# Kernel tuning notes

Measured on AMD Instinct MI355X. Metric: run time of the kernel, lower is better.

Reference implementation:

```python
import jax, jax.numpy as jnp
import numpy as np

N_NODES = 100000
N_EDGES = 1600000
D_IN = 256
D_OUT = 128


def setup_inputs() -> dict:
    key = jax.random.key(0)
    k1, k2, k3, k4, k5, k6 = jax.random.split(key, 6)
    inp = {
        "input": jax.random.normal(k1, (N_NODES, D_IN), dtype=jnp.float32),
        "edge_row": jax.random.randint(k2, (N_EDGES,), 0, N_NODES),
        "edge_col": jax.random.randint(k3, (N_EDGES,), 0, N_NODES),
        "edge_val": jax.random.uniform(k4, (N_EDGES,), dtype=jnp.float32),
        "W": jax.random.normal(k5, (D_IN, D_OUT), dtype=jnp.float32) * (1.0 / np.sqrt(D_IN)),
        "b": jax.random.normal(k6, (D_OUT,), dtype=jnp.float32) * 0.01,
    }
    return inp


def reference(input, edge_row, edge_col, edge_val, W, b):
    # support = Linear(input)  -> [N, D_OUT]
    support = jnp.dot(input, W) + b
    # sparse.mm(adj, support): out[r] = sum_e val[e] * support[col[e]] for edges with row[e]==r
    msgs = edge_val[:, None] * support[edge_col]  # [E, D_OUT]
    agg = jax.ops.segment_sum(msgs, edge_row, num_segments=N_NODES)  # [N, D_OUT]
    return jnp.tanh(agg)
```

## Files before the change

kernel.cpp:

```cpp
#include <hip/hip_runtime.h>
#include <math.h>

#define N_NODES 100000
#define N_EDGES 1600000
#define D_IN 256
#define D_OUT 128

#define OFF_SUPPORT 0
#define OFF_COUNTS  51200000
#define OFF_CSREV   51600008
#define OFF_BSUMS   64400008
#define OFF_WTHI    64400416
#define OFF_WTLO    64465952

#define SCAN_CHUNK  1024
#define SCAN_BLOCKS ((N_NODES + SCAN_CHUNK - 1) / SCAN_CHUNK)

#define GB 128
#define GEMM_BLOCKS ((N_NODES + GB - 1) / GB)
#define EDGE_BLOCKS ((N_EDGES + 255) / 256)

typedef __attribute__((ext_vector_type(8))) short s8v;
typedef __attribute__((ext_vector_type(4))) float f4v;

__device__ __forceinline__ short f2bf(float x) {
  unsigned u = __float_as_uint(x);
  unsigned r = u + 0x7FFF + ((u >> 16) & 1);
  return (short)(r >> 16);
}
__device__ __forceinline__ float bf2f(short h) {
  return __uint_as_float(((unsigned)(unsigned short)h) << 16);
}

__device__ __forceinline__ void cvt8(float4 a, float4 b, s8v& h, s8v& l) {
  float f[8] = {a.x, a.y, a.z, a.w, b.x, b.y, b.z, b.w};
#pragma unroll
  for (int i = 0; i < 8; i++) {
    short hh = f2bf(f[i]);
    h[i] = hh;
    l[i] = f2bf(f[i] - bf2f(hh));
  }
}

typedef const float __attribute__((address_space(1)))* gas1f;
typedef float __attribute__((address_space(3)))* las3f;
__device__ __forceinline__ void gload_lds16(const float* g, float* l) {
  __builtin_amdgcn_global_load_lds((gas1f)g, (las3f)l, 16, 0, 0);
}

__global__ __launch_bounds__(256) void wconv_kernel(
    const float* __restrict__ W, short* __restrict__ wt_hi,
    short* __restrict__ wt_lo, int* __restrict__ counts) {
  int idx = blockIdx.x * 256 + threadIdx.x;
  int k = idx >> 7;
  int n = idx & 127;
  float v = W[idx];
  short h = f2bf(v);
  wt_hi[n * 256 + k] = h;
  wt_lo[n * 256 + k] = f2bf(v - bf2f(h));
  for (int i = idx; i < N_NODES + 1; i += 32768) counts[i] = 0;
}

__device__ __forceinline__ void gemm_body(
    int gb, const float* __restrict__ input, const short* __restrict__ wt_hi,
    const short* __restrict__ wt_lo, const float* __restrict__ b,
    float* __restrict__ support) {
  __shared__ float Af[4][2][32][32];
  const int t = threadIdx.x;
  const int lane = t & 63;
  const int wv = t >> 6;
  const int qm = lane & 15;
  const int quad = lane >> 4;
  const int node0 = gb * GB;

  const int srow = lane >> 3;
  const int gc = (lane & 7) ^ srow;

  auto stage = [&](int kt, int buf) {
#pragma unroll
    for (int j = 0; j < 4; ++j) {
      int nd = node0 + wv * 32 + j * 8 + srow;
      if (nd > N_NODES - 1) nd = N_NODES - 1;
      gload_lds16(input + (size_t)nd * D_IN + kt * 32 + gc * 4,
                  &Af[wv][buf][j * 8][0]);
    }
  };

  stage(0, 0);
  stage(1, 1);

  f4v acc[2][8];
#pragma unroll
  for (int mt = 0; mt < 2; mt++)
#pragma unroll
    for (int nt = 0; nt < 8; nt++) acc[mt][nt] = (f4v){0.f, 0.f, 0.f, 0.f};

  const int p0 = (2 * quad) ^ (qm & 7);
  const int p1 = (2 * quad + 1) ^ (qm & 7);

#pragma unroll
  for (int kt = 0; kt < 8; ++kt) {
    const int cb = kt & 1;
    asm volatile("s_waitcnt vmcnt(4)" ::: "memory");
    float4 x00 = *(const float4*)&Af[wv][cb][qm][p0 * 4];
    float4 x01 = *(const float4*)&Af[wv][cb][qm][p1 * 4];
    float4 x10 = *(const float4*)&Af[wv][cb][qm + 16][p0 * 4];
    float4 x11 = *(const float4*)&Af[wv][cb][qm + 16][p1 * 4];
    asm volatile("s_waitcnt lgkmcnt(0)" ::: "memory");
    __builtin_amdgcn_sched_barrier(0);

    const int koff = kt * 32 + quad * 8;
    s8v bh[8], bl[8];
#pragma unroll
    for (int nt = 0; nt < 8; ++nt) {
      size_t bo = (size_t)(nt * 16 + qm) * 256 + koff;
      bh[nt] = *(const s8v*)(wt_hi + bo);
      bl[nt] = *(const s8v*)(wt_lo + bo);
    }
    __builtin_amdgcn_sched_barrier(0);
    if (kt < 6) stage(kt + 2, cb);
    __builtin_amdgcn_sched_barrier(0);

    s8v ah0, al0, ah1, al1;
    cvt8(x00, x01, ah0, al0);
    cvt8(x10, x11, ah1, al1);
#pragma unroll
    for (int nt = 0; nt < 8; ++nt) {
      acc[0][nt] = __builtin_amdgcn_mfma_f32_16x16x32_bf16(ah0, bh[nt], acc[0][nt], 0, 0, 0);
      acc[0][nt] = __builtin_amdgcn_mfma_f32_16x16x32_bf16(ah0, bl[nt], acc[0][nt], 0, 0, 0);
      acc[0][nt] = __builtin_amdgcn_mfma_f32_16x16x32_bf16(al0, bh[nt], acc[0][nt], 0, 0, 0);
      acc[1][nt] = __builtin_amdgcn_mfma_f32_16x16x32_bf16(ah1, bh[nt], acc[1][nt], 0, 0, 0);
      acc[1][nt] = __builtin_amdgcn_mfma_f32_16x16x32_bf16(ah1, bl[nt], acc[1][nt], 0, 0, 0);
      acc[1][nt] = __builtin_amdgcn_mfma_f32_16x16x32_bf16(al1, bh[nt], acc[1][nt], 0, 0, 0);
    }
  }

  float bias[8];
#pragma unroll
  for (int nt = 0; nt < 8; nt++) bias[nt] = b[nt * 16 + qm];
#pragma unroll
  for (int mt = 0; mt < 2; mt++) {
#pragma unroll
    for (int nt = 0; nt < 8; nt++) {
      int col = nt * 16 + qm;
#pragma unroll
      for (int r = 0; r < 4; r++) {
        int node = node0 + wv * 32 + mt * 16 + quad * 4 + r;
        if (node < N_NODES)
          support[(size_t)node * D_OUT + col] = acc[mt][nt][r] + bias[nt];
      }
    }
  }
}

__global__ __launch_bounds__(256, 2) void gemm_hist_kernel(
    const float* __restrict__ input, const short* __restrict__ wt_hi,
    const short* __restrict__ wt_lo, const float* __restrict__ b,
    float* __restrict__ support, const int* __restrict__ erow,
    int* __restrict__ counts, int* __restrict__ pos_e) {
  if (blockIdx.x < GEMM_BLOCKS) {
    gemm_body(blockIdx.x, input, wt_hi, wt_lo, b, support);
  } else {
    int e = (blockIdx.x - GEMM_BLOCKS) * 256 + threadIdx.x;
    if (e < N_EDGES) pos_e[e] = atomicAdd(&counts[erow[e]], 1);
  }
}

__global__ __launch_bounds__(256) void build_kernel(
    const int* __restrict__ erow, const int* __restrict__ ecol,
    const float* __restrict__ eval, const int* __restrict__ offsets,
    const int* __restrict__ pos_e, int2* __restrict__ csr_ev) {
  int e = blockIdx.x * 256 + threadIdx.x;
  if (e < N_EDGES) {
    int idx = offsets[erow[e]] + pos_e[e];
    csr_ev[idx] = make_int2(ecol[e], __float_as_int(eval[e]));
  }
}

__global__ __launch_bounds__(256) void scan_phase1(const int* __restrict__ counts,
                                                   int* __restrict__ bsums) {
  __shared__ int ts[256];
  int t = threadIdx.x;
  int idx0 = blockIdx.x * SCAN_CHUNK + t * 4;
  int s = 0;
#pragma unroll
  for (int i = 0; i < 4; i++)
    if (idx0 + i < N_NODES) s += counts[idx0 + i];
  ts[t] = s;
  __syncthreads();
#pragma unroll
  for (int off = 128; off > 0; off >>= 1) {
    if (t < off) ts[t] += ts[t + off];
    __syncthreads();
  }
  if (t == 0) bsums[blockIdx.x] = ts[0];
}

__global__ __launch_bounds__(128) void scan_phase2(int* __restrict__ bsums) {
  __shared__ int s[128];
  int t = threadIdx.x;
  int v = (t < SCAN_BLOCKS) ? bsums[t] : 0;
  s[t] = v;
  __syncthreads();
#pragma unroll
  for (int off = 1; off < 128; off <<= 1) {
    int x = (t >= off) ? s[t - off] : 0;
    __syncthreads();
    s[t] += x;
    __syncthreads();
  }
  if (t < SCAN_BLOCKS) bsums[t] = s[t] - v;
}

__global__ __launch_bounds__(256) void scan_phase3(int* __restrict__ counts,
                                                   const int* __restrict__ bsums) {
  __shared__ int ts[256];
  int t = threadIdx.x;
  int b = blockIdx.x;
  int idx0 = b * SCAN_CHUNK + t * 4;
  int v[4];
  int s = 0;
#pragma unroll
  for (int i = 0; i < 4; i++) {
    v[i] = (idx0 + i < N_NODES) ? counts[idx0 + i] : 0;
    s += v[i];
  }
  ts[t] = s;
  __syncthreads();
#pragma unroll
  for (int off = 1; off < 256; off <<= 1) {
    int x = (t >= off) ? ts[t - off] : 0;
    __syncthreads();
    ts[t] += x;
    __syncthreads();
  }
  int run = bsums[b] + ts[t] - s;
#pragma unroll
  for (int i = 0; i < 4; i++) {
    int idx = idx0 + i;
    if (idx < N_NODES) counts[idx] = run;
    run += v[i];
  }
  if (b == 0 && t == 0) counts[N_NODES] = N_EDGES;
}

__global__ __launch_bounds__(256) void agg_kernel(
    const int* __restrict__ offsets, const int2* __restrict__ csr_ev,
    const float* __restrict__ support, float* __restrict__ out) {
  int r = blockIdx.x * 8 + (threadIdx.x >> 5);
  int l4 = (threadIdx.x & 31) * 4;
  int beg = offsets[r];
  int end = offsets[r + 1];
  float4 acc = make_float4(0.f, 0.f, 0.f, 0.f);

  if (end > beg) {
    int2 e[8], en[8];
#pragma unroll
    for (int u = 0; u < 8; u++) {
      int idx = beg + u;
      int c = idx < end ? idx : end - 1;
      e[u] = csr_ev[c];
      if (idx >= end) e[u].y = 0;
    }
    for (int j = beg; j < end; j += 8) {
      int jn = j + 8;
      if (jn < end) {
#pragma unroll
        for (int u = 0; u < 8; u++) {
          int idx = jn + u;
          int c = idx < end ? idx : end - 1;
          en[u] = csr_ev[c];
          if (idx >= end) en[u].y = 0;
        }
      }
      float4 s[8];
#pragma unroll
      for (int u = 0; u < 8; u++)
        s[u] = *(const float4*)(support + (size_t)e[u].x * D_OUT + l4);
#pragma unroll
      for (int u = 0; u < 8; u++) {
        float v = __int_as_float(e[u].y);
        acc.x = fmaf(v, s[u].x, acc.x);
        acc.y = fmaf(v, s[u].y, acc.y);
        acc.z = fmaf(v, s[u].z, acc.z);
        acc.w = fmaf(v, s[u].w, acc.w);
      }
#pragma unroll
      for (int u = 0; u < 8; u++) e[u] = en[u];
    }
  }
  *(float4*)(out + (size_t)r * D_OUT + l4) =
      make_float4(tanhf(acc.x), tanhf(acc.y), tanhf(acc.z), tanhf(acc.w));
}

extern "C" void kernel_launch(void* const* d_in, const int* in_sizes, int n_in,
                              void* d_out, int out_size, void* d_ws, size_t ws_size,
                              hipStream_t stream) {
  const float* input = (const float*)d_in[0];
  const int* erow = (const int*)d_in[1];
  const int* ecol = (const int*)d_in[2];
  const float* eval = (const float*)d_in[3];
  const float* W = (const float*)d_in[4];
  const float* b = (const float*)d_in[5];
  float* out = (float*)d_out;

  char* ws = (char*)d_ws;
  float* support = (float*)(ws + OFF_SUPPORT);
  int* counts = (int*)(ws + OFF_COUNTS);
  int2* csr_ev = (int2*)(ws + OFF_CSREV);
  int* bsums = (int*)(ws + OFF_BSUMS);
  short* wt_hi = (short*)(ws + OFF_WTHI);
  short* wt_lo = (short*)(ws + OFF_WTLO);
  int* pos_e = (int*)d_out;

  hipLaunchKernelGGL(wconv_kernel, dim3((D_IN * D_OUT) / 256), dim3(256), 0,
                     stream, W, wt_hi, wt_lo, counts);

  hipLaunchKernelGGL(gemm_hist_kernel, dim3(GEMM_BLOCKS + EDGE_BLOCKS),
                     dim3(256), 0, stream, input, wt_hi, wt_lo, b, support,
                     erow, counts, pos_e);
  hipLaunchKernelGGL(scan_phase1, dim3(SCAN_BLOCKS), dim3(256), 0, stream,
                     counts, bsums);
  hipLaunchKernelGGL(scan_phase2, dim3(1), dim3(128), 0, stream, bsums);
  hipLaunchKernelGGL(scan_phase3, dim3(SCAN_BLOCKS), dim3(256), 0, stream,
                     counts, bsums);
  hipLaunchKernelGGL(build_kernel, dim3(EDGE_BLOCKS), dim3(256), 0, stream,
                     erow, ecol, eval, counts, pos_e, csr_ev);
  hipLaunchKernelGGL(agg_kernel, dim3(N_NODES / 8), dim3(256), 0, stream,
                     counts, csr_ev, support, out);
}
```

Before: 438.2 us.

## Split histogram from GEMM and compute CSR slots with atomics in build

Moves the edge-row histogram out of the fused GEMM kernel into a prep kernel alongside the W conversion. The per-edge position array is dropped, so build_kernel now assigns CSR slots through a second atomic counter that scan_phase3 zeroes. The counts array is cleared with a memset, and the GEMM kernel's launch bound goes from 2 to 3 blocks per SM. The aim is to keep the histogram atomics from contending with the GEMM and to raise GEMM occupancy. In exchange, build does an extra atomic per edge, it is an extra launch, and edge order within each row becomes nondeterministic, so float summation order can vary between runs.

```diff
diff --git a/kernel.cpp b/kernel.cpp
--- a/kernel.cpp
+++ b/kernel.cpp
@@ -19,6 +19,7 @@
 #define GB 128
 #define GEMM_BLOCKS ((N_NODES + GB - 1) / GB)
 #define EDGE_BLOCKS ((N_EDGES + 255) / 256)
+#define WCONV_BLOCKS ((D_IN * D_OUT) / 256)
 
 typedef __attribute__((ext_vector_type(8))) short s8v;
 typedef __attribute__((ext_vector_type(4))) float f4v;
@@ -48,17 +49,22 @@
   __builtin_amdgcn_global_load_lds((gas1f)g, (las3f)l, 16, 0, 0);
 }
 
-__global__ __launch_bounds__(256) void wconv_kernel(
+__global__ __launch_bounds__(256) void prep_kernel(
     const float* __restrict__ W, short* __restrict__ wt_hi,
-    short* __restrict__ wt_lo, int* __restrict__ counts) {
-  int idx = blockIdx.x * 256 + threadIdx.x;
-  int k = idx >> 7;
-  int n = idx & 127;
-  float v = W[idx];
-  short h = f2bf(v);
-  wt_hi[n * 256 + k] = h;
-  wt_lo[n * 256 + k] = f2bf(v - bf2f(h));
-  for (int i = idx; i < N_NODES + 1; i += 32768) counts[i] = 0;
+    short* __restrict__ wt_lo, const int* __restrict__ erow,
+    int* __restrict__ counts) {
+  if (blockIdx.x < WCONV_BLOCKS) {
+    int idx = blockIdx.x * 256 + threadIdx.x;
+    int k = idx >> 7;
+    int n = idx & 127;
+    float v = W[idx];
+    short h = f2bf(v);
+    wt_hi[n * 256 + k] = h;
+    wt_lo[n * 256 + k] = f2bf(v - bf2f(h));
+  } else {
+    int e = (blockIdx.x - WCONV_BLOCKS) * 256 + threadIdx.x;
+    if (e < N_EDGES) atomicAdd(&counts[erow[e]], 1);
+  }
 }
 
 __device__ __forceinline__ void gemm_body(
@@ -153,26 +159,21 @@
   }
 }
 
-__global__ __launch_bounds__(256, 2) void gemm_hist_kernel(
+__global__ __launch_bounds__(256, 3) void gemm_kernel(
     const float* __restrict__ input, const short* __restrict__ wt_hi,
     const short* __restrict__ wt_lo, const float* __restrict__ b,
-    float* __restrict__ support, const int* __restrict__ erow,
-    int* __restrict__ counts, int* __restrict__ pos_e) {
-  if (blockIdx.x < GEMM_BLOCKS) {
-    gemm_body(blockIdx.x, input, wt_hi, wt_lo, b, support);
-  } else {
-    int e = (blockIdx.x - GEMM_BLOCKS) * 256 + threadIdx.x;
-    if (e < N_EDGES) pos_e[e] = atomicAdd(&counts[erow[e]], 1);
-  }
+    float* __restrict__ support) {
+  gemm_body(blockIdx.x, input, wt_hi, wt_lo, b, support);
 }
 
 __global__ __launch_bounds__(256) void build_kernel(
     const int* __restrict__ erow, const int* __restrict__ ecol,
     const float* __restrict__ eval, const int* __restrict__ offsets,
-    const int* __restrict__ pos_e, int2* __restrict__ csr_ev) {
+    int* __restrict__ fill, int2* __restrict__ csr_ev) {
   int e = blockIdx.x * 256 + threadIdx.x;
   if (e < N_EDGES) {
-    int idx = offsets[erow[e]] + pos_e[e];
+    int r = erow[e];
+    int idx = offsets[r] + atomicAdd(&fill[r], 1);
     csr_ev[idx] = make_int2(ecol[e], __float_as_int(eval[e]));
   }
 }
@@ -213,7 +214,8 @@
 }
 
 __global__ __launch_bounds__(256) void scan_phase3(int* __restrict__ counts,
-                                                   const int* __restrict__ bsums) {
+                                                   const int* __restrict__ bsums,
+                                                   int* __restrict__ fill) {
   __shared__ int ts[256];
   int t = threadIdx.x;
   int b = blockIdx.x;
@@ -238,7 +240,10 @@
 #pragma unroll
   for (int i = 0; i < 4; i++) {
     int idx = idx0 + i;
-    if (idx < N_NODES) counts[idx] = run;
+    if (idx < N_NODES) {
+      counts[idx] = run;
+      fill[idx] = 0;
+    }
     run += v[i];
   }
   if (b == 0 && t == 0) counts[N_NODES] = N_EDGES;
@@ -311,21 +316,21 @@
   int* bsums = (int*)(ws + OFF_BSUMS);
   short* wt_hi = (short*)(ws + OFF_WTHI);
   short* wt_lo = (short*)(ws + OFF_WTLO);
-  int* pos_e = (int*)d_out;
-
-  hipLaunchKernelGGL(wconv_kernel, dim3((D_IN * D_OUT) / 256), dim3(256), 0,
-                     stream, W, wt_hi, wt_lo, counts);
-
-  hipLaunchKernelGGL(gemm_hist_kernel, dim3(GEMM_BLOCKS + EDGE_BLOCKS),
-                     dim3(256), 0, stream, input, wt_hi, wt_lo, b, support,
-                     erow, counts, pos_e);
+  int* fill = (int*)d_out;
+
+  hipMemsetAsync(ws + OFF_COUNTS, 0, (size_t)(N_NODES + 1) * 4, stream);
+
+  hipLaunchKernelGGL(prep_kernel, dim3(WCONV_BLOCKS + EDGE_BLOCKS), dim3(256),
+                     0, stream, W, wt_hi, wt_lo, erow, counts);
+  hipLaunchKernelGGL(gemm_kernel, dim3(GEMM_BLOCKS), dim3(256), 0, stream,
+                     input, wt_hi, wt_lo, b, support);
   hipLaunchKernelGGL(scan_phase1, dim3(SCAN_BLOCKS), dim3(256), 0, stream,
                      counts, bsums);
   hipLaunchKernelGGL(scan_phase2, dim3(1), dim3(128), 0, stream, bsums);
   hipLaunchKernelGGL(scan_phase3, dim3(SCAN_BLOCKS), dim3(256), 0, stream,
-                     counts, bsums);
+                     counts, bsums, fill);
   hipLaunchKernelGGL(build_kernel, dim3(EDGE_BLOCKS), dim3(256), 0, stream,
-                     erow, ecol, eval, counts, pos_e, csr_ev);
+                     erow, ecol, eval, counts, fill, csr_ev);
   hipLaunchKernelGGL(agg_kernel, dim3(N_NODES / 8), dim3(256), 0, stream,
                      counts, csr_ev, support, out);
 }
```

Result: slower. 528.1 us (+20.5%).
